# Kernel optimization log

Hardware: AMD Instinct MI355X
Metric: run time of the kernel (lower is better)

Reference implementation:

```python
import jax, jax.numpy as jnp
import numpy as np

HEADS = 8
HEAD_DIM = 64
INNER = HEADS * HEAD_DIM  # 512
DIM = 512
B, H, W = 8, 32, 32
KV_LEN, KV_DIM = 77, 1024


def group_norm(x, g, b, groups=32, eps=1e-6):
    # x: [B, C, H, W]
    Bx, C, Hx, Wx = x.shape
    xr = x.reshape(Bx, groups, C // groups, Hx, Wx)
    mu = xr.mean(axis=(2, 3, 4), keepdims=True)
    var = xr.var(axis=(2, 3, 4), keepdims=True)
    xr = (xr - mu) * jax.lax.rsqrt(var + eps)
    return xr.reshape(Bx, C, Hx, Wx) * g[None, :, None, None] + b[None, :, None, None]


def layer_norm(x, g, b, eps=1e-5):
    mu = x.mean(axis=-1, keepdims=True)
    var = x.var(axis=-1, keepdims=True)
    return (x - mu) * jax.lax.rsqrt(var + eps) * g + b


def attention(qx, kvx, Wq, Wk, Wv, Wo, bo):
    # qx: [B, Sq, dim_q], kvx: [B, Sk, dim_kv]
    q = qx @ Wq
    k = kvx @ Wk
    v = kvx @ Wv
    Bx, Sq, _ = q.shape
    Sk = k.shape[1]
    q = q.reshape(Bx, Sq, HEADS, HEAD_DIM)
    k = k.reshape(Bx, Sk, HEADS, HEAD_DIM)
    v = v.reshape(Bx, Sk, HEADS, HEAD_DIM)
    att = jnp.einsum('bqhd,bkhd->bhqk', q, k) * (HEAD_DIM ** -0.5)
    att = jax.nn.softmax(att.astype(jnp.float32), axis=-1).astype(q.dtype)
    o = jnp.einsum('bhqk,bkhd->bqhd', att, v).reshape(Bx, Sq, INNER)
    return o @ Wo + bo


def setup_inputs() -> dict:
    key = jax.random.key(0)
    ks = jax.random.split(key, 20)
    s = 0.02
    def n(k, shape):
        return jax.random.normal(k, shape, jnp.float32) * s
    return {
        'q': jax.random.normal(ks[0], (B, DIM, H, W), jnp.float32),
        'kv': jax.random.normal(ks[1], (B, KV_LEN, KV_DIM), jnp.float32),
        'gn_g': jnp.ones((DIM,), jnp.float32), 'gn_b': jnp.zeros((DIM,), jnp.float32),
        'ln2_g': jnp.ones((INNER,), jnp.float32), 'ln2_b': jnp.zeros((INNER,), jnp.float32),
        'ln3_g': jnp.ones((INNER,), jnp.float32), 'ln3_b': jnp.zeros((INNER,), jnp.float32),
        'ln4_g': jnp.ones((INNER,), jnp.float32), 'ln4_b': jnp.zeros((INNER,), jnp.float32),
        'fc_in_w': n(ks[2], (DIM, INNER)), 'fc_in_b': jnp.zeros((INNER,), jnp.float32),
        'fc_out_w': n(ks[3], (INNER, DIM)), 'fc_out_b': jnp.zeros((DIM,), jnp.float32),
        'a1_q': n(ks[4], (INNER, INNER)), 'a1_k': n(ks[5], (INNER, INNER)),
        'a1_v': n(ks[6], (INNER, INNER)), 'a1_o': n(ks[7], (INNER, INNER)),
        'a1_ob': jnp.zeros((INNER,), jnp.float32),
        'a2_q': n(ks[8], (INNER, INNER)), 'a2_k': n(ks[9], (KV_DIM, INNER)),
        'a2_v': n(ks[10], (KV_DIM, INNER)), 'a2_o': n(ks[11], (INNER, INNER)),
        'a2_ob': jnp.zeros((INNER,), jnp.float32),
        'ff_proj_w': n(ks[12], (INNER, INNER * 8)), 'ff_proj_b': jnp.zeros((INNER * 8,), jnp.float32),
        'ff_out_w': n(ks[13], (INNER * 4, INNER)), 'ff_out_b': jnp.zeros((INNER,), jnp.float32),
    }


def reference(q, kv, gn_g, gn_b, ln2_g, ln2_b, ln3_g, ln3_b, ln4_g, ln4_b,
              fc_in_w, fc_in_b, fc_out_w, fc_out_b,
              a1_q, a1_k, a1_v, a1_o, a1_ob,
              a2_q, a2_k, a2_v, a2_o, a2_ob,
              ff_proj_w, ff_proj_b, ff_out_w, ff_out_b):
    res = q
    Bx, C, Hx, Wx = q.shape
    x = group_norm(q, gn_g, gn_b)
    x = x.reshape(Bx, C, Hx * Wx).transpose(0, 2, 1)  # [B, S, C]
    x = x @ fc_in_w + fc_in_b
    t = layer_norm(x, ln2_g, ln2_b)
    x = attention(t, t, a1_q, a1_k, a1_v, a1_o, a1_ob) + x
    x = attention(layer_norm(x, ln3_g, ln3_b), kv, a2_q, a2_k, a2_v, a2_o, a2_ob) + x
    h = layer_norm(x, ln4_g, ln4_b) @ ff_proj_w + ff_proj_b
    a, gate = jnp.split(h, 2, axis=-1)
    x = (a * jax.nn.gelu(gate, approximate=False)) @ ff_out_w + ff_out_b + x
    x = x @ fc_out_w + fc_out_b
    x = x.transpose(0, 2, 1).reshape(Bx, C, Hx, Wx)
    return x + res
```

## Files before the change

### kernel.cpp

```cpp
#include <hip/hip_runtime.h>
#include <cstdint>
#include <cstddef>

typedef __attribute__((ext_vector_type(8))) short bf16x8;
typedef __attribute__((ext_vector_type(4))) short short4v;
typedef __attribute__((ext_vector_type(4))) float f32x4;

__device__ __forceinline__ short f2b(float f) {
    unsigned u = __builtin_bit_cast(unsigned, f);
    u = (u + 0x7FFFu + ((u >> 16) & 1u)) >> 16;
    return (short)u;
}
__device__ __forceinline__ float b2f(short s) {
    unsigned u = ((unsigned)(unsigned short)s) << 16;
    return __builtin_bit_cast(float, u);
}

__device__ __forceinline__ void gload16(const short* g, short* l) {
    __builtin_amdgcn_global_load_lds(
        (const __attribute__((address_space(1))) unsigned int*)g,
        (__attribute__((address_space(3))) unsigned int*)l, 16, 0, 0);
}

__device__ __forceinline__ float gelu_fast(float g) {
    float g2 = g * g;
    float gp = g * (0.7978845608f + 0.0356774081f * g2);
    float t = exp2f(-2.885390082f * gp);
    return g / (1.f + t);
}

__device__ __forceinline__ int pn_ffp(int n) {
    int m = (n < 2048) ? n : (n - 2048);
    int gofs = (n < 2048) ? 0 : 32;
    int x = m >> 6, c = m & 63;
    return x * 128 + ((c >> 5) << 6) + gofs + (c & 31);
}

struct PrepArgs {
    const float* src[12];
    short* dst[12];
    const float* kv;
    short* kvb;
    const float* fb;
    float* bp;
};

__global__ __launch_bounds__(256) void prep(PrepArgs a) {
    int t = blockIdx.x;
    int tid = threadIdx.x;
    if (t >= 6144) {
        if (t >= 6452) {
            int n = (t - 6452) * 256 + tid;
            if (n < 4096) a.bp[pn_ffp(n)] = a.fb[n];
            return;
        }
        int idx = (t - 6144) * 256 + tid;
        if (idx >= 78848) return;
        const float4* s = (const float4*)a.kv + (size_t)idx * 2;
        float4 va = s[0], vb = s[1];
        bf16x8 w;
        w[0] = f2b(va.x); w[1] = f2b(va.y); w[2] = f2b(va.z); w[3] = f2b(va.w);
        w[4] = f2b(vb.x); w[5] = f2b(vb.y); w[6] = f2b(vb.z); w[7] = f2b(vb.w);
        *(bf16x8*)(a.kvb + (size_t)idx * 8) = w;
        return;
    }
    const int jstart[12] = {0, 256, 512, 768, 1024, 1280, 1536, 1792, 2304, 2816, 3072, 5120};
    const int jK[12] = {512, 512, 512, 512, 512, 512, 512, 1024, 1024, 512, 512, 2048};
    const int jN[12] = {512, 512, 512, 512, 512, 512, 512, 512, 512, 512, 4096, 512};
    int j = 11;
#pragma unroll
    for (int i = 11; i >= 1; --i)
        if (t < jstart[i]) j = i - 1;
    int tx = t - jstart[j];
    int K = jK[j], N = jN[j];
    int tn = N >> 5;
    int n0 = (tx % tn) * 32, k0 = (tx / tn) * 32;
    const float* w = a.src[j];
    short* wt = a.dst[j];
    bool perm = (j == 10);

    __shared__ float tile[32][33];
    int cx = tid & 31, ty0 = tid >> 5;
#pragma unroll
    for (int i = 0; i < 4; ++i) {
        int r = ty0 + i * 8;
        tile[r][cx] = w[(size_t)(k0 + r) * N + n0 + cx];
    }
    __syncthreads();
    int r = tid >> 3;
    int kg = (tid & 7) * 4;
    int drow = perm ? pn_ffp(n0 + r) : (n0 + r);
    short4v o = {f2b(tile[kg][r]), f2b(tile[kg + 1][r]),
                 f2b(tile[kg + 2][r]), f2b(tile[kg + 3][r])};
    *(short4v*)&wt[(size_t)drow * K + k0 + kg] = o;
}

__global__ __launch_bounds__(256) void gn_stats(const float* __restrict__ q,
                                                const float* __restrict__ g,
                                                const float* __restrict__ bta,
                                                float* __restrict__ sc,
                                                float* __restrict__ sh) {
    int bb = blockIdx.x >> 5, gg = blockIdx.x & 31;
    const float4* src = (const float4*)(q + ((size_t)(bb * 512 + gg * 16)) * 1024);
    float s = 0.f, s2 = 0.f;
#pragma unroll
    for (int i = 0; i < 16; ++i) {
        float4 v = src[threadIdx.x + 256 * i];
        s += (v.x + v.y) + (v.z + v.w);
        s2 += (v.x * v.x + v.y * v.y) + (v.z * v.z + v.w * v.w);
    }
#pragma unroll
    for (int m = 1; m < 64; m <<= 1) {
        s += __shfl_xor(s, m);
        s2 += __shfl_xor(s2, m);
    }
    __shared__ float red[8];
    int wv = threadIdx.x >> 6;
    if ((threadIdx.x & 63) == 0) { red[wv] = s; red[4 + wv] = s2; }
    __syncthreads();
    if (threadIdx.x < 16) {
        float S = red[0] + red[1] + red[2] + red[3];
        float S2 = red[4] + red[5] + red[6] + red[7];
        float mu = S * (1.f / 16384.f);
        float var = S2 * (1.f / 16384.f) - mu * mu;
        float rs = rsqrtf(var + 1e-6f);
        int c = gg * 16 + threadIdx.x;
        float scale = rs * g[c];
        sc[bb * 512 + c] = scale;
        sh[bb * 512 + c] = bta[c] - mu * scale;
    }
}

__global__ __launch_bounds__(256) void gn_apply(const float* __restrict__ q,
                                                const float* __restrict__ sc,
                                                const float* __restrict__ sh,
                                                short* __restrict__ out) {
    __shared__ short tile[512][33];
    int b = blockIdx.x >> 5, st = blockIdx.x & 31;
    int s0 = st * 32;
    int sl = threadIdx.x & 31, cg = threadIdx.x >> 5;
    for (int c = cg; c < 512; c += 8) {
        float v = q[((size_t)(b * 512 + c)) * 1024 + s0 + sl];
        float y = v * sc[b * 512 + c] + sh[b * 512 + c];
        tile[c][sl] = f2b(y);
    }
    __syncthreads();
    int sr = threadIdx.x >> 3, ch = threadIdx.x & 7;
    short* orow = out + ((size_t)(b * 1024 + s0 + sr)) * 512;
    for (int c8 = ch * 64; c8 < ch * 64 + 64; c8 += 8) {
        bf16x8 o;
#pragma unroll
        for (int jj = 0; jj < 8; ++jj) o[jj] = tile[c8 + jj][sr];
        *(bf16x8*)&orow[c8] = o;
    }
}

__global__ __launch_bounds__(256) void ln_rows(const short* __restrict__ x,
                                               const float* __restrict__ g,
                                               const float* __restrict__ bta,
                                               short* __restrict__ out) {
    int row = blockIdx.x * 4 + (threadIdx.x >> 6);
    int lane = threadIdx.x & 63;
    bf16x8 v8 = *(const bf16x8*)(x + (size_t)row * 512 + lane * 8);
    float v[8];
#pragma unroll
    for (int j = 0; j < 8; ++j) v[j] = b2f(v8[j]);
    float s = 0.f, s2 = 0.f;
#pragma unroll
    for (int j = 0; j < 8; ++j) { s += v[j]; s2 += v[j] * v[j]; }
#pragma unroll
    for (int m = 1; m < 64; m <<= 1) {
        s += __shfl_xor(s, m);
        s2 += __shfl_xor(s2, m);
    }
    float mu = s * (1.f / 512.f);
    float var = s2 * (1.f / 512.f) - mu * mu;
    float rs = rsqrtf(var + 1e-5f);
    float4 ga = ((const float4*)g)[lane * 2], gb = ((const float4*)g)[lane * 2 + 1];
    float4 ba = ((const float4*)bta)[lane * 2], bb = ((const float4*)bta)[lane * 2 + 1];
    bf16x8 o;
    o[0] = f2b((v[0] - mu) * rs * ga.x + ba.x);
    o[1] = f2b((v[1] - mu) * rs * ga.y + ba.y);
    o[2] = f2b((v[2] - mu) * rs * ga.z + ba.z);
    o[3] = f2b((v[3] - mu) * rs * ga.w + ba.w);
    o[4] = f2b((v[4] - mu) * rs * gb.x + bb.x);
    o[5] = f2b((v[5] - mu) * rs * gb.y + bb.y);
    o[6] = f2b((v[6] - mu) * rs * gb.z + bb.z);
    o[7] = f2b((v[7] - mu) * rs * gb.w + bb.w);
    *(bf16x8*)(out + (size_t)row * 512 + lane * 8) = o;
}

template <int BN>
__global__ __launch_bounds__(256, 1) void gemm_gl(
    const short* __restrict__ A, const short* __restrict__ BT,
    int M, int N, int K,
    const float* __restrict__ bias,
    const short* __restrict__ addSrcB,
    short* __restrict__ outB,
    const float* __restrict__ resid,
    float* __restrict__ outFinal,
    int mode) {
    constexpr int FJ = BN / 32;
    constexpr int ASZ = 3 * 128 * 32;
    constexpr int BSZ = 3 * BN * 32;
    __shared__ __attribute__((aligned(16))) short smem[ASZ + BSZ];
    short* Asb = smem;
    short* Bsb = smem + ASZ;
    int tid = threadIdx.x;
    int wave = tid >> 6, lane = tid & 63;
    int wr = wave >> 1, wc = wave & 1;
    int m0 = blockIdx.y * 128, n0 = blockIdx.x * BN;
    f32x4 acc[4][FJ];
#pragma unroll
    for (int i = 0; i < 4; ++i)
#pragma unroll
        for (int j = 0; j < FJ; ++j) acc[i][j] = (f32x4){0.f, 0.f, 0.f, 0.f};

    int srow = tid >> 2;
    int scg = (((tid & 3) ^ ((tid >> 3) & 3)) << 3);
    int ar0 = m0 + srow; if (ar0 >= M) ar0 = M - 1;
    int ar1 = m0 + 64 + srow; if (ar1 >= M) ar1 = M - 1;
    const short* ag0 = A + (size_t)ar0 * K + scg;
    const short* ag1 = A + (size_t)ar1 * K + scg;
    const short* bg0 = BT + (size_t)(n0 + srow) * K + scg;
    const short* bg1 = BT + (size_t)(n0 + 64 + srow) * K + scg;
    int nk = K >> 5;

    auto stage = [&](int buf) {
        gload16(ag0, &Asb[buf * 4096 + wave * 512]);
        gload16(ag1, &Asb[buf * 4096 + 2048 + wave * 512]);
        gload16(bg0, &Bsb[buf * (BN * 32) + wave * 512]);
        if constexpr (BN == 128) gload16(bg1, &Bsb[buf * 4096 + 2048 + wave * 512]);
        ag0 += 32; ag1 += 32; bg0 += 32; bg1 += 32;
    };
    stage(0);
    stage(1);

    int lr = lane & 15, g = lane >> 4;

#define GL_STEP(KT, BUF)                                                          \
    {                                                                             \
        __builtin_amdgcn_sched_barrier(0);                                        \
        if ((KT) + 1 < nk) {                                                      \
            if constexpr (BN == 128)                                              \
                asm volatile("s_waitcnt vmcnt(4)" ::: "memory");                  \
            else                                                                  \
                asm volatile("s_waitcnt vmcnt(3)" ::: "memory");                  \
        } else {                                                                  \
            asm volatile("s_waitcnt vmcnt(0)" ::: "memory");                      \
        }                                                                         \
        __builtin_amdgcn_sched_barrier(0);                                        \
        __builtin_amdgcn_s_barrier();                                             \
        if ((KT) + 2 < nk) stage(((BUF) + 2) % 3);                                \
        bf16x8 af[4], bfr[FJ];                                                    \
        _Pragma("unroll") for (int i = 0; i < 4; ++i) {                           \
            int row = wr * 64 + i * 16 + lr;                                      \
            af[i] = *(const bf16x8*)&Asb[(BUF) * 4096 + row * 32 +                \
                                         ((g ^ ((row >> 1) & 3)) << 3)];          \
        }                                                                         \
        _Pragma("unroll") for (int j = 0; j < FJ; ++j) {                          \
            int row = wc * (BN / 2) + j * 16 + lr;                                \
            bfr[j] = *(const bf16x8*)&Bsb[(BUF) * (BN * 32) + row * 32 +          \
                                          ((g ^ ((row >> 1) & 3)) << 3)];         \
        }                                                                         \
        _Pragma("unroll") for (int i = 0; i < 4; ++i)                             \
            _Pragma("unroll") for (int j = 0; j < FJ; ++j)                        \
                acc[i][j] = __builtin_amdgcn_mfma_f32_16x16x32_bf16(              \
                    af[i], bfr[j], acc[i][j], 0, 0, 0);                           \
    }

    for (int kt = 0; kt < nk; kt += 3) {
        GL_STEP(kt, 0);
        if (kt + 1 < nk) GL_STEP(kt + 1, 1);
        if (kt + 2 < nk) GL_STEP(kt + 2, 2);
    }
#undef GL_STEP

    int lq = lane >> 4;
    if (mode == 1) {
#pragma unroll
        for (int i = 0; i < 4; ++i)
#pragma unroll
            for (int j = 0; j < FJ; ++j) {
                int mm0 = m0 + wr * 64 + i * 16 + lq * 4;
                int nn = n0 + wc * (BN / 2) + j * 16 + lr;
                int bb = mm0 >> 10, ss = mm0 & 1023;
                size_t oi = ((size_t)(bb * 512 + nn)) * 1024 + ss;
                float bv = bias ? bias[nn] : 0.f;
                float4 rv = *(const float4*)&resid[oi];
                float4 ov;
                ov.x = acc[i][j][0] + bv + rv.x;
                ov.y = acc[i][j][1] + bv + rv.y;
                ov.z = acc[i][j][2] + bv + rv.z;
                ov.w = acc[i][j][3] + bv + rv.w;
                *(float4*)&outFinal[oi] = ov;
            }
        return;
    }
    {
        constexpr int EC = BN + 4;
        float* ef = (float*)smem;
#pragma unroll
        for (int h = 0; h < 2; ++h) {
            __syncthreads();
            if (wr == h) {
#pragma unroll
                for (int i = 0; i < 4; ++i)
#pragma unroll
                    for (int j = 0; j < FJ; ++j)
#pragma unroll
                        for (int r = 0; r < 4; ++r)
                            ef[(i * 16 + lq * 4 + r) * EC + wc * (BN / 2) + j * 16 + lr] =
                                acc[i][j][r];
            }
            __syncthreads();
#pragma unroll
            for (int q = 0; q < BN / 16; ++q) {
                int idx = q * 256 + tid;
                int row = idx / (BN / 4);
                int cq = (idx % (BN / 4)) * 4;
                int mm = m0 + h * 64 + row;
                if (mm >= M) continue;
                int nn = n0 + cq;
                float4 v = *(float4*)&ef[row * EC + cq];
                if (bias) {
                    float4 b4 = *(const float4*)&bias[nn];
                    v.x += b4.x; v.y += b4.y; v.z += b4.z; v.w += b4.w;
                }
                size_t ig = (size_t)mm * N + nn;
                if (addSrcB) {
                    short4v a4 = *(const short4v*)&addSrcB[ig];
                    v.x += b2f(a4[0]); v.y += b2f(a4[1]);
                    v.z += b2f(a4[2]); v.w += b2f(a4[3]);
                }
                short4v o = {f2b(v.x), f2b(v.y), f2b(v.z), f2b(v.w)};
                *(short4v*)&outB[ig] = o;
            }
        }
    }
}

__global__ __launch_bounds__(512, 1) void gemm256w(
    const short* __restrict__ A, const short* __restrict__ BT,
    int M, int N, int K,
    const float* __restrict__ bias,
    const short* __restrict__ addSrcB,
    short* __restrict__ outB,
    int mode) {
    __shared__ __attribute__((aligned(16))) short smem[3 * 4096 + 3 * 8192];
    short* Asb = smem;
    short* Bsb = smem + 12288;
    int tid = threadIdx.x;
    int wave = tid >> 6, lane = tid & 63;
    int wrM = wave >> 2, wcN = wave & 3;
    int m0 = blockIdx.y * 128, n0 = blockIdx.x * 256;
    f32x4 acc[4][4];
#pragma unroll
    for (int i = 0; i < 4; ++i)
#pragma unroll
        for (int j = 0; j < 4; ++j) acc[i][j] = (f32x4){0.f, 0.f, 0.f, 0.f};

    const short* gp[3];
    int ldsoff[3];
    bool isA[3];
#pragma unroll
    for (int s = 0; s < 3; ++s) {
        int qq = wave * 3 + s;
        bool a = qq < 8;
        int r = (a ? qq : qq - 8) * 16 + (lane >> 2);
        int sc = (((lane & 3) ^ ((r >> 1) & 3)) << 3);
        gp[s] = a ? (A + (size_t)(m0 + r) * K + sc)
                  : (BT + (size_t)(n0 + r) * K + sc);
        ldsoff[s] = (a ? qq : (qq - 8)) * 512;
        isA[s] = a;
    }
    int nk = K >> 5;
    auto stage = [&](int buf) {
#pragma unroll
        for (int s = 0; s < 3; ++s) {
            short* l = isA[s] ? &Asb[buf * 4096 + ldsoff[s]]
                              : &Bsb[buf * 8192 + ldsoff[s]];
            gload16(gp[s], l);
            gp[s] += 32;
        }
    };
    stage(0);
    stage(1);

    int lr = lane & 15, g = lane >> 4;

#define W8_STEP(KT, BUF)                                                          \
    {                                                                             \
        __builtin_amdgcn_sched_barrier(0);                                        \
        if ((KT) + 1 < nk) {                                                      \
            asm volatile("s_waitcnt vmcnt(3)" ::: "memory");                      \
        } else {                                                                  \
            asm volatile("s_waitcnt vmcnt(0)" ::: "memory");                      \
        }                                                                         \
        __builtin_amdgcn_sched_barrier(0);                                        \
        __builtin_amdgcn_s_barrier();                                             \
        if ((KT) + 2 < nk) stage(((BUF) + 2) % 3);                                \
        bf16x8 af[4], bfr[4];                                                     \
        _Pragma("unroll") for (int i = 0; i < 4; ++i) {                           \
            int row = wrM * 64 + i * 16 + lr;                                     \
            af[i] = *(const bf16x8*)&Asb[(BUF) * 4096 + row * 32 +                \
                                         ((g ^ ((row >> 1) & 3)) << 3)];          \
        }                                                                         \
        _Pragma("unroll") for (int j = 0; j < 4; ++j) {                           \
            int row = wcN * 64 + j * 16 + lr;                                     \
            bfr[j] = *(const bf16x8*)&Bsb[(BUF) * 8192 + row * 32 +               \
                                          ((g ^ ((row >> 1) & 3)) << 3)];         \
        }                                                                         \
        _Pragma("unroll") for (int i = 0; i < 4; ++i)                             \
            _Pragma("unroll") for (int j = 0; j < 4; ++j)                         \
                acc[i][j] = __builtin_amdgcn_mfma_f32_16x16x32_bf16(              \
                    af[i], bfr[j], acc[i][j], 0, 0, 0);                           \
    }

    for (int kt = 0; kt < nk; kt += 3) {
        W8_STEP(kt, 0);
        if (kt + 1 < nk) W8_STEP(kt + 1, 1);
        if (kt + 2 < nk) W8_STEP(kt + 2, 2);
    }
#undef W8_STEP

    int lq = lane >> 4;
    if (mode == 2) {
        short* eb = smem;
        int xhalf = wcN >> 1, half = wcN & 1;
        __syncthreads();
#pragma unroll
        for (int i = 0; i < 4; ++i)
#pragma unroll
            for (int j = 0; j < 2; ++j)
#pragma unroll
                for (int r = 0; r < 4; ++r) {
                    int slot = n0 + wcN * 64 + j * 16 + lr;
                    float a = acc[i][j][r] + bias[slot];
                    float gt = acc[i][j + 2][r] + bias[slot + 32];
                    float ge = gelu_fast(gt);
                    int row = wrM * 64 + i * 16 + lq * 4 + r;
                    int col = xhalf * 64 + half * 32 + j * 16 + lr;
                    eb[row * 136 + col] = f2b(a * ge);
                }
        __syncthreads();
#pragma unroll
        for (int q = 0; q < 4; ++q) {
            int idx = q * 512 + tid;
            int row = idx >> 4, cg = (idx & 15) * 8;
            bf16x8 o = *(bf16x8*)&eb[row * 136 + cg];
            *(bf16x8*)&outB[(size_t)(m0 + row) * 2048 + blockIdx.x * 128 + cg] = o;
        }
        return;
    }
    {
        float* ef = (float*)smem;
#pragma unroll
        for (int h = 0; h < 2; ++h) {
            __syncthreads();
            if (wrM == h) {
#pragma unroll
                for (int i = 0; i < 4; ++i)
#pragma unroll
                    for (int j = 0; j < 4; ++j)
#pragma unroll
                        for (int r = 0; r < 4; ++r)
                            ef[(i * 16 + lq * 4 + r) * 260 + wcN * 64 + j * 16 + lr] =
                                acc[i][j][r];
            }
            __syncthreads();
#pragma unroll
            for (int q = 0; q < 8; ++q) {
                int idx = q * 512 + tid;
                int row = idx >> 6;
                int cq = (idx & 63) * 4;
                float4 v = *(float4*)&ef[row * 260 + cq];
                int nn = n0 + cq;
                if (bias) {
                    float4 b4 = *(const float4*)&bias[nn];
                    v.x += b4.x; v.y += b4.y; v.z += b4.z; v.w += b4.w;
                }
                size_t ig = (size_t)(m0 + h * 64 + row) * N + nn;
                if (addSrcB) {
                    short4v a4 = *(const short4v*)&addSrcB[ig];
                    v.x += b2f(a4[0]); v.y += b2f(a4[1]);
                    v.z += b2f(a4[2]); v.w += b2f(a4[3]);
                }
                short4v o = {f2b(v.x), f2b(v.y), f2b(v.z), f2b(v.w)};
                *(short4v*)&outB[ig] = o;
            }
        }
    }
}

__global__ __launch_bounds__(256, 1) void attn_mfma(const short* __restrict__ qp,
                                                    const short* __restrict__ kp,
                                                    const short* __restrict__ vp,
                                                    short* __restrict__ op,
                                                    int kv_len, int kvBatchRows,
                                                    int qStride, int kvStride) {
    __shared__ __attribute__((aligned(16))) short Kt[64][72];
    __shared__ __attribute__((aligned(16))) short Vt[64][72];
    __shared__ __attribute__((aligned(16))) short Pt[4][2][16][72];
    int tid = threadIdx.x, w = tid >> 6, lane = tid & 63;
    int g = lane >> 4, c = lane & 15;
    int id = blockIdx.x;
    int xcd = id & 7, jj2 = id >> 3;
    int bh = xcd * 8 + (jj2 >> 3);
    int qtile = jj2 & 7;
    int b = bh >> 3, h = bh & 7;
    int q0 = qtile * 128 + w * 16;

    const float QS = 0.125f * 1.44269504f;
    bf16x8 qa[2][2];
#pragma unroll
    for (int qi = 0; qi < 2; ++qi) {
        const short* qbase = qp + ((size_t)(b * 1024 + q0 + qi * 64 + c)) * qStride + h * 64;
        bf16x8 qr0 = *(const bf16x8*)(qbase + g * 8);
        bf16x8 qr1 = *(const bf16x8*)(qbase + 32 + g * 8);
#pragma unroll
        for (int j = 0; j < 8; ++j) {
            qa[qi][0][j] = f2b(b2f(qr0[j]) * QS);
            qa[qi][1][j] = f2b(b2f(qr1[j]) * QS);
        }
    }

    f32x4 oac[2][4];
#pragma unroll
    for (int qi = 0; qi < 2; ++qi)
#pragma unroll
        for (int dt = 0; dt < 4; ++dt) oac[qi][dt] = (f32x4){0.f, 0.f, 0.f, 0.f};
    float l[2][4];
#pragma unroll
    for (int qi = 0; qi < 2; ++qi)
#pragma unroll
        for (int r = 0; r < 4; ++r) l[qi][r] = 0.f;

    int skey = tid & 63, sd0 = (tid >> 6) * 16;
    int ntile = (kv_len + 63) >> 6;
    size_t kvbase = (size_t)b * kvBatchRows;

    bf16x8 k0, k1, v0, v1;
    {
        int krow = skey < kv_len ? skey : kv_len - 1;
        const short* kpp = kp + (kvbase + krow) * kvStride + h * 64 + sd0;
        const short* vpp = vp + (kvbase + krow) * kvStride + h * 64 + sd0;
        k0 = *(const bf16x8*)kpp; k1 = *(const bf16x8*)(kpp + 8);
        v0 = *(const bf16x8*)vpp; v1 = *(const bf16x8*)(vpp + 8);
    }

    for (int kt = 0; kt < ntile; ++kt) {
        __syncthreads();
        *(bf16x8*)&Kt[skey][sd0] = k0;
        *(bf16x8*)&Kt[skey][sd0 + 8] = k1;
#pragma unroll
        for (int j = 0; j < 8; ++j) {
            Vt[sd0 + j][skey] = v0[j];
            Vt[sd0 + 8 + j][skey] = v1[j];
        }
        __syncthreads();
        if (kt + 1 < ntile) {
            int krow = (kt + 1) * 64 + skey;
            if (krow >= kv_len) krow = kv_len - 1;
            const short* kpp = kp + (kvbase + krow) * kvStride + h * 64 + sd0;
            const short* vpp = vp + (kvbase + krow) * kvStride + h * 64 + sd0;
            k0 = *(const bf16x8*)kpp; k1 = *(const bf16x8*)(kpp + 8);
            v0 = *(const bf16x8*)vpp; v1 = *(const bf16x8*)(vpp + 8);
        }

        f32x4 s[2][4];
        __builtin_amdgcn_s_setprio(1);
#pragma unroll
        for (int nt = 0; nt < 4; ++nt) {
            bf16x8 kb0 = *(const bf16x8*)&Kt[nt * 16 + c][g * 8];
            bf16x8 kb1 = *(const bf16x8*)&Kt[nt * 16 + c][32 + g * 8];
#pragma unroll
            for (int qi = 0; qi < 2; ++qi) {
                s[qi][nt] = __builtin_amdgcn_mfma_f32_16x16x32_bf16(
                    qa[qi][0], kb0, (f32x4){0.f, 0.f, 0.f, 0.f}, 0, 0, 0);
                s[qi][nt] = __builtin_amdgcn_mfma_f32_16x16x32_bf16(
                    qa[qi][1], kb1, s[qi][nt], 0, 0, 0);
            }
        }
        __builtin_amdgcn_s_setprio(0);
        if (kt * 64 + 64 > kv_len) {
#pragma unroll
            for (int nt = 0; nt < 4; ++nt) {
                bool valid = kt * 64 + nt * 16 + c < kv_len;
#pragma unroll
                for (int qi = 0; qi < 2; ++qi)
#pragma unroll
                    for (int r = 0; r < 4; ++r) {
                        float pv = valid ? exp2f(s[qi][nt][r]) : 0.f;
                        s[qi][nt][r] = pv;
                        l[qi][r] += pv;
                    }
            }
        } else {
#pragma unroll
            for (int nt = 0; nt < 4; ++nt)
#pragma unroll
                for (int qi = 0; qi < 2; ++qi)
#pragma unroll
                    for (int r = 0; r < 4; ++r) {
                        float pv = exp2f(s[qi][nt][r]);
                        s[qi][nt][r] = pv;
                        l[qi][r] += pv;
                    }
        }

        bf16x8 pa[2][2];
#pragma unroll
        for (int qi = 0; qi < 2; ++qi) {
#pragma unroll
            for (int nt = 0; nt < 4; ++nt)
#pragma unroll
                for (int r = 0; r < 4; ++r)
                    Pt[w][qi][4 * g + r][nt * 16 + c] = f2b(s[qi][nt][r]);
        }
#pragma unroll
        for (int qi = 0; qi < 2; ++qi) {
            pa[qi][0] = *(const bf16x8*)&Pt[w][qi][c][g * 8];
            pa[qi][1] = *(const bf16x8*)&Pt[w][qi][c][32 + g * 8];
        }
        __builtin_amdgcn_s_setprio(1);
#pragma unroll
        for (int dt = 0; dt < 4; ++dt) {
            bf16x8 vb0 = *(const bf16x8*)&Vt[dt * 16 + c][g * 8];
            bf16x8 vb1 = *(const bf16x8*)&Vt[dt * 16 + c][32 + g * 8];
#pragma unroll
            for (int qi = 0; qi < 2; ++qi) {
                oac[qi][dt] = __builtin_amdgcn_mfma_f32_16x16x32_bf16(pa[qi][0], vb0, oac[qi][dt], 0, 0, 0);
                oac[qi][dt] = __builtin_amdgcn_mfma_f32_16x16x32_bf16(pa[qi][1], vb1, oac[qi][dt], 0, 0, 0);
            }
        }
        __builtin_amdgcn_s_setprio(0);
    }

#pragma unroll
    for (int mk = 1; mk < 16; mk <<= 1)
#pragma unroll
        for (int qi = 0; qi < 2; ++qi)
#pragma unroll
            for (int r = 0; r < 4; ++r) l[qi][r] += __shfl_xor(l[qi][r], mk);
#pragma unroll
    for (int qi = 0; qi < 2; ++qi)
#pragma unroll
        for (int r = 0; r < 4; ++r) {
            float inv = 1.f / l[qi][r];
            short* orow = op + ((size_t)(b * 1024 + q0 + qi * 64 + 4 * g + r)) * 512 + h * 64;
#pragma unroll
            for (int dt = 0; dt < 4; ++dt)
                orow[dt * 16 + c] = f2b(oac[qi][dt][r] * inv);
        }
}

extern "C" void kernel_launch(void* const* d_in, const int* in_sizes, int n_in,
                              void* d_out, int out_size, void* d_ws, size_t ws_size,
                              hipStream_t stream) {
    (void)in_sizes; (void)n_in; (void)out_size; (void)ws_size;
    const float* q_in = (const float*)d_in[0];
    const float* kv_in = (const float*)d_in[1];
    const float* gn_g = (const float*)d_in[2];
    const float* gn_b = (const float*)d_in[3];
    const float* ln2_g = (const float*)d_in[4];
    const float* ln2_b = (const float*)d_in[5];
    const float* ln3_g = (const float*)d_in[6];
    const float* ln3_b = (const float*)d_in[7];
    const float* ln4_g = (const float*)d_in[8];
    const float* ln4_b = (const float*)d_in[9];
    const float* fc_in_w = (const float*)d_in[10];
    const float* fc_in_b = (const float*)d_in[11];
    const float* fc_out_w = (const float*)d_in[12];
    const float* fc_out_b = (const float*)d_in[13];
    const float* a1_qw = (const float*)d_in[14];
    const float* a1_kw = (const float*)d_in[15];
    const float* a1_vw = (const float*)d_in[16];
    const float* a1_ow = (const float*)d_in[17];
    const float* a1_ob = (const float*)d_in[18];
    const float* a2_qw = (const float*)d_in[19];
    const float* a2_kw = (const float*)d_in[20];
    const float* a2_vw = (const float*)d_in[21];
    const float* a2_ow = (const float*)d_in[22];
    const float* a2_ob = (const float*)d_in[23];
    const float* ffp_w = (const float*)d_in[24];
    const float* ffp_b = (const float*)d_in[25];
    const float* ffo_w = (const float*)d_in[26];
    const float* ffo_b = (const float*)d_in[27];
    float* out = (float*)d_out;

    char* p = (char*)d_ws;
    auto alloc = [&](size_t n) {
        char* r = p;
        p += (n + 255) & ~(size_t)255;
        return r;
    };
    short* wt_fci = (short*)alloc((size_t)512 * 512 * 2);
    short* wt_fco = (short*)alloc((size_t)512 * 512 * 2);
    short* wt_qkv = (short*)alloc((size_t)1536 * 512 * 2);
    short* wt_a1o = (short*)alloc((size_t)512 * 512 * 2);
    short* wt_a2q = (short*)alloc((size_t)512 * 512 * 2);
    short* wt_kv2 = (short*)alloc((size_t)1024 * 1024 * 2);
    short* wt_a2o = (short*)alloc((size_t)512 * 512 * 2);
    short* wt_ffp = (short*)alloc((size_t)4096 * 512 * 2);
    short* wt_ffo = (short*)alloc((size_t)512 * 2048 * 2);
    float* biasP = (float*)alloc((size_t)4096 * 4);
    short* xb = (short*)alloc((size_t)8192 * 512 * 2);
    short* tb = (short*)alloc((size_t)8192 * 512 * 2);
    short* qkvbuf = (short*)alloc((size_t)8192 * 1536 * 2);
    short* qbuf = (short*)alloc((size_t)8192 * 512 * 2);
    short* kvpbuf = (short*)alloc((size_t)616 * 1024 * 2);
    short* obuf = (short*)alloc((size_t)8192 * 512 * 2);
    short* kvb = (short*)alloc((size_t)616 * 1024 * 2);
    short* ggb = (short*)alloc((size_t)8192 * 2048 * 2);
    float* gnsc = (float*)alloc((size_t)8 * 512 * 4);
    float* gnsh = (float*)alloc((size_t)8 * 512 * 4);

    PrepArgs pa;
    pa.src[0] = fc_in_w;  pa.dst[0] = wt_fci;
    pa.src[1] = fc_out_w; pa.dst[1] = wt_fco;
    pa.src[2] = a1_qw;    pa.dst[2] = wt_qkv;
    pa.src[3] = a1_kw;    pa.dst[3] = wt_qkv + (size_t)512 * 512;
    pa.src[4] = a1_vw;    pa.dst[4] = wt_qkv + (size_t)1024 * 512;
    pa.src[5] = a1_ow;    pa.dst[5] = wt_a1o;
    pa.src[6] = a2_qw;    pa.dst[6] = wt_a2q;
    pa.src[7] = a2_kw;    pa.dst[7] = wt_kv2;
    pa.src[8] = a2_vw;    pa.dst[8] = wt_kv2 + (size_t)512 * 1024;
    pa.src[9] = a2_ow;    pa.dst[9] = wt_a2o;
    pa.src[10] = ffp_w;   pa.dst[10] = wt_ffp;
    pa.src[11] = ffo_w;   pa.dst[11] = wt_ffo;
    pa.kv = kv_in; pa.kvb = kvb; pa.fb = ffp_b; pa.bp = biasP;
    prep<<<6468, 256, 0, stream>>>(pa);

    auto gemm128n = [&](const short* A, const short* BT, int M, int N, int K,
                        const float* bias, const short* addSrcB, short* outB,
                        const float* resid, float* outFinal, int mode) {
        dim3 g(N / 128, (M + 127) / 128);
        gemm_gl<128><<<g, 256, 0, stream>>>(A, BT, M, N, K, bias, addSrcB, outB,
                                            resid, outFinal, mode);
    };

    gn_stats<<<256, 256, 0, stream>>>(q_in, gn_g, gn_b, gnsc, gnsh);
    gn_apply<<<256, 256, 0, stream>>>(q_in, gnsc, gnsh, tb);
    gemm128n(tb, wt_fci, 8192, 512, 512, fc_in_b, nullptr, xb, nullptr, nullptr, 0);
    ln_rows<<<2048, 256, 0, stream>>>(xb, ln2_g, ln2_b, tb);
    gemm256w<<<dim3(6, 64), 512, 0, stream>>>(tb, wt_qkv, 8192, 1536, 512,
                                              nullptr, nullptr, qkvbuf, 0);
    attn_mfma<<<512, 256, 0, stream>>>(qkvbuf, qkvbuf + 512, qkvbuf + 1024, obuf,
                                       1024, 1024, 1536, 1536);
    gemm128n(obuf, wt_a1o, 8192, 512, 512, a1_ob, xb, xb, nullptr, nullptr, 0);
    ln_rows<<<2048, 256, 0, stream>>>(xb, ln3_g, ln3_b, tb);
    gemm128n(tb, wt_a2q, 8192, 512, 512, nullptr, nullptr, qbuf, nullptr, nullptr, 0);
    gemm128n(kvb, wt_kv2, 616, 1024, 1024, nullptr, nullptr, kvpbuf, nullptr, nullptr, 0);
    attn_mfma<<<512, 256, 0, stream>>>(qbuf, kvpbuf, kvpbuf + 512, obuf,
                                       77, 77, 512, 1024);
    gemm128n(obuf, wt_a2o, 8192, 512, 512, a2_ob, xb, xb, nullptr, nullptr, 0);
    ln_rows<<<2048, 256, 0, stream>>>(xb, ln4_g, ln4_b, tb);
    gemm256w<<<dim3(16, 64), 512, 0, stream>>>(tb, wt_ffp, 8192, 4096, 512,
                                               biasP, nullptr, ggb, 2);
    gemm256w<<<dim3(2, 64), 512, 0, stream>>>(ggb, wt_ffo, 8192, 512, 2048,
                                              ffo_b, xb, tb, 0);
    gemm128n(tb, wt_fco, 8192, 512, 512, fc_out_b, nullptr, nullptr, q_in, out, 1);
}
```

Baseline: 294.6 us.

## Fold GN stats into prep, template GEMM K, compute softmax sum via MFMA

The group-norm statistics kernel is merged into the prep launch as extra blocks, which removes one kernel launch. The GEMM kernels now take K as a template parameter and fully unroll the k-loop, so the compiler can specialize addressing. In attention, the per-row softmax denominator is now accumulated with extra MFMAs against a vector of bf16 ones, replacing scalar adds and cross-lane shuffles. The denominator is then summed from bf16-rounded probabilities, and the fully unrolled loops increase code size.

```diff
diff --git a/kernel.cpp b/kernel.cpp
--- a/kernel.cpp
+++ b/kernel.cpp
@@ -43,12 +43,50 @@
     short* kvb;
     const float* fb;
     float* bp;
+    const float* qin;
+    const float* gng;
+    const float* gnb;
+    float* gnsc;
+    float* gnsh;
 };
 
 __global__ __launch_bounds__(256) void prep(PrepArgs a) {
     int t = blockIdx.x;
     int tid = threadIdx.x;
+    __shared__ float tile[32][33];
     if (t >= 6144) {
+        if (t >= 6468) {
+            int bb = (t - 6468) >> 5, gg = (t - 6468) & 31;
+            const float4* src = (const float4*)(a.qin + ((size_t)(bb * 512 + gg * 16)) * 1024);
+            float s = 0.f, s2 = 0.f;
+#pragma unroll
+            for (int i = 0; i < 16; ++i) {
+                float4 v = src[tid + 256 * i];
+                s += (v.x + v.y) + (v.z + v.w);
+                s2 += (v.x * v.x + v.y * v.y) + (v.z * v.z + v.w * v.w);
+            }
+#pragma unroll
+            for (int m = 1; m < 64; m <<= 1) {
+                s += __shfl_xor(s, m);
+                s2 += __shfl_xor(s2, m);
+            }
+            float* red = &tile[0][0];
+            int wv = tid >> 6;
+            if ((tid & 63) == 0) { red[wv] = s; red[4 + wv] = s2; }
+            __syncthreads();
+            if (tid < 16) {
+                float S = red[0] + red[1] + red[2] + red[3];
+                float S2 = red[4] + red[5] + red[6] + red[7];
+                float mu = S * (1.f / 16384.f);
+                float var = S2 * (1.f / 16384.f) - mu * mu;
+                float rs = rsqrtf(var + 1e-6f);
+                int c = gg * 16 + tid;
+                float scale = rs * a.gng[c];
+                a.gnsc[bb * 512 + c] = scale;
+                a.gnsh[bb * 512 + c] = a.gnb[c] - mu * scale;
+            }
+            return;
+        }
         if (t >= 6452) {
             int n = (t - 6452) * 256 + tid;
             if (n < 4096) a.bp[pn_ffp(n)] = a.fb[n];
@@ -79,7 +117,6 @@
     short* wt = a.dst[j];
     bool perm = (j == 10);
 
-    __shared__ float tile[32][33];
     int cx = tid & 31, ty0 = tid >> 5;
 #pragma unroll
     for (int i = 0; i < 4; ++i) {
@@ -93,42 +130,6 @@
     short4v o = {f2b(tile[kg][r]), f2b(tile[kg + 1][r]),
                  f2b(tile[kg + 2][r]), f2b(tile[kg + 3][r])};
     *(short4v*)&wt[(size_t)drow * K + k0 + kg] = o;
-}
-
-__global__ __launch_bounds__(256) void gn_stats(const float* __restrict__ q,
-                                                const float* __restrict__ g,
-                                                const float* __restrict__ bta,
-                                                float* __restrict__ sc,
-                                                float* __restrict__ sh) {
-    int bb = blockIdx.x >> 5, gg = blockIdx.x & 31;
-    const float4* src = (const float4*)(q + ((size_t)(bb * 512 + gg * 16)) * 1024);
-    float s = 0.f, s2 = 0.f;
-#pragma unroll
-    for (int i = 0; i < 16; ++i) {
-        float4 v = src[threadIdx.x + 256 * i];
-        s += (v.x + v.y) + (v.z + v.w);
-        s2 += (v.x * v.x + v.y * v.y) + (v.z * v.z + v.w * v.w);
-    }
-#pragma unroll
-    for (int m = 1; m < 64; m <<= 1) {
-        s += __shfl_xor(s, m);
-        s2 += __shfl_xor(s2, m);
-    }
-    __shared__ float red[8];
-    int wv = threadIdx.x >> 6;
-    if ((threadIdx.x & 63) == 0) { red[wv] = s; red[4 + wv] = s2; }
-    __syncthreads();
-    if (threadIdx.x < 16) {
-        float S = red[0] + red[1] + red[2] + red[3];
-        float S2 = red[4] + red[5] + red[6] + red[7];
-        float mu = S * (1.f / 16384.f);
-        float var = S2 * (1.f / 16384.f) - mu * mu;
-        float rs = rsqrtf(var + 1e-6f);
-        int c = gg * 16 + threadIdx.x;
-        float scale = rs * g[c];
-        sc[bb * 512 + c] = scale;
-        sh[bb * 512 + c] = bta[c] - mu * scale;
-    }
 }
 
 __global__ __launch_bounds__(256) void gn_apply(const float* __restrict__ q,
@@ -190,10 +191,10 @@
     *(bf16x8*)(out + (size_t)row * 512 + lane * 8) = o;
 }
 
-template <int BN>
+template <int BN, int KK>
 __global__ __launch_bounds__(256, 1) void gemm_gl(
     const short* __restrict__ A, const short* __restrict__ BT,
-    int M, int N, int K,
+    int M, int N,
     const float* __restrict__ bias,
     const short* __restrict__ addSrcB,
     short* __restrict__ outB,
@@ -201,6 +202,8 @@
     float* __restrict__ outFinal,
     int mode) {
     constexpr int FJ = BN / 32;
+    constexpr int K = KK;
+    constexpr int nk = KK / 32;
     constexpr int ASZ = 3 * 128 * 32;
     constexpr int BSZ = 3 * BN * 32;
     __shared__ __attribute__((aligned(16))) short smem[ASZ + BSZ];
@@ -224,7 +227,6 @@
     const short* ag1 = A + (size_t)ar1 * K + scg;
     const short* bg0 = BT + (size_t)(n0 + srow) * K + scg;
     const short* bg1 = BT + (size_t)(n0 + 64 + srow) * K + scg;
-    int nk = K >> 5;
 
     auto stage = [&](int buf) {
         gload16(ag0, &Asb[buf * 4096 + wave * 512]);
@@ -269,6 +271,7 @@
                     af[i], bfr[j], acc[i][j], 0, 0, 0);                           \
     }
 
+#pragma unroll
     for (int kt = 0; kt < nk; kt += 3) {
         GL_STEP(kt, 0);
         if (kt + 1 < nk) GL_STEP(kt + 1, 1);
@@ -340,13 +343,16 @@
     }
 }
 
+template <int KK>
 __global__ __launch_bounds__(512, 1) void gemm256w(
     const short* __restrict__ A, const short* __restrict__ BT,
-    int M, int N, int K,
+    int M, int N,
     const float* __restrict__ bias,
     const short* __restrict__ addSrcB,
     short* __restrict__ outB,
     int mode) {
+    constexpr int K = KK;
+    constexpr int nk = KK / 32;
     __shared__ __attribute__((aligned(16))) short smem[3 * 4096 + 3 * 8192];
     short* Asb = smem;
     short* Bsb = smem + 12288;
@@ -374,7 +380,6 @@
         ldsoff[s] = (a ? qq : (qq - 8)) * 512;
         isA[s] = a;
     }
-    int nk = K >> 5;
     auto stage = [&](int buf) {
 #pragma unroll
         for (int s = 0; s < 3; ++s) {
@@ -417,6 +422,7 @@
                     af[i], bfr[j], acc[i][j], 0, 0, 0);                           \
     }
 
+#pragma unroll
     for (int kt = 0; kt < nk; kt += 3) {
         W8_STEP(kt, 0);
         if (kt + 1 < nk) W8_STEP(kt + 1, 1);
@@ -524,17 +530,17 @@
             qa[qi][1][j] = f2b(b2f(qr1[j]) * QS);
         }
     }
-
-    f32x4 oac[2][4];
-#pragma unroll
-    for (int qi = 0; qi < 2; ++qi)
+    bf16x8 vones;
+#pragma unroll
+    for (int j = 0; j < 8; ++j) vones[j] = (short)0x3F80;
+
+    f32x4 oac[2][4], oacl[2];
+#pragma unroll
+    for (int qi = 0; qi < 2; ++qi) {
 #pragma unroll
         for (int dt = 0; dt < 4; ++dt) oac[qi][dt] = (f32x4){0.f, 0.f, 0.f, 0.f};
-    float l[2][4];
-#pragma unroll
-    for (int qi = 0; qi < 2; ++qi)
-#pragma unroll
-        for (int r = 0; r < 4; ++r) l[qi][r] = 0.f;
+        oacl[qi] = (f32x4){0.f, 0.f, 0.f, 0.f};
+    }
 
     int skey = tid & 63, sd0 = (tid >> 6) * 16;
     int ntile = (kv_len + 63) >> 6;
@@ -590,11 +596,8 @@
 #pragma unroll
                 for (int qi = 0; qi < 2; ++qi)
 #pragma unroll
-                    for (int r = 0; r < 4; ++r) {
-                        float pv = valid ? exp2f(s[qi][nt][r]) : 0.f;
-                        s[qi][nt][r] = pv;
-                        l[qi][r] += pv;
-                    }
+                    for (int r = 0; r < 4; ++r)
+                        s[qi][nt][r] = valid ? exp2f(s[qi][nt][r]) : 0.f;
             }
         } else {
 #pragma unroll
@@ -602,11 +605,8 @@
 #pragma unroll
                 for (int qi = 0; qi < 2; ++qi)
 #pragma unroll
-                    for (int r = 0; r < 4; ++r) {
-                        float pv = exp2f(s[qi][nt][r]);
-                        s[qi][nt][r] = pv;
-                        l[qi][r] += pv;
-                    }
+                    for (int r = 0; r < 4; ++r)
+                        s[qi][nt][r] = exp2f(s[qi][nt][r]);
         }
 
         bf16x8 pa[2][2];
@@ -634,20 +634,19 @@
                 oac[qi][dt] = __builtin_amdgcn_mfma_f32_16x16x32_bf16(pa[qi][1], vb1, oac[qi][dt], 0, 0, 0);
             }
         }
+#pragma unroll
+        for (int qi = 0; qi < 2; ++qi) {
+            oacl[qi] = __builtin_amdgcn_mfma_f32_16x16x32_bf16(pa[qi][0], vones, oacl[qi], 0, 0, 0);
+            oacl[qi] = __builtin_amdgcn_mfma_f32_16x16x32_bf16(pa[qi][1], vones, oacl[qi], 0, 0, 0);
+        }
         __builtin_amdgcn_s_setprio(0);
     }
 
 #pragma unroll
-    for (int mk = 1; mk < 16; mk <<= 1)
-#pragma unroll
-        for (int qi = 0; qi < 2; ++qi)
-#pragma unroll
-            for (int r = 0; r < 4; ++r) l[qi][r] += __shfl_xor(l[qi][r], mk);
-#pragma unroll
     for (int qi = 0; qi < 2; ++qi)
 #pragma unroll
         for (int r = 0; r < 4; ++r) {
-            float inv = 1.f / l[qi][r];
+            float inv = 1.f / oacl[qi][r];
             short* orow = op + ((size_t)(b * 1024 + q0 + qi * 64 + 4 * g + r)) * 512 + h * 64;
 #pragma unroll
             for (int dt = 0; dt < 4; ++dt)
@@ -730,35 +729,33 @@
     pa.src[10] = ffp_w;   pa.dst[10] = wt_ffp;
     pa.src[11] = ffo_w;   pa.dst[11] = wt_ffo;
     pa.kv = kv_in; pa.kvb = kvb; pa.fb = ffp_b; pa.bp = biasP;
-    prep<<<6468, 256, 0, stream>>>(pa);
-
-    auto gemm128n = [&](const short* A, const short* BT, int M, int N, int K,
-                        const float* bias, const short* addSrcB, short* outB,
-                        const float* resid, float* outFinal, int mode) {
-        dim3 g(N / 128, (M + 127) / 128);
-        gemm_gl<128><<<g, 256, 0, stream>>>(A, BT, M, N, K, bias, addSrcB, outB,
-                                            resid, outFinal, mode);
-    };
-
-    gn_stats<<<256, 256, 0, stream>>>(q_in, gn_g, gn_b, gnsc, gnsh);
+    pa.qin = q_in; pa.gng = gn_g; pa.gnb = gn_b; pa.gnsc = gnsc; pa.gnsh = gnsh;
+    prep<<<6724, 256, 0, stream>>>(pa);
+
     gn_apply<<<256, 256, 0, stream>>>(q_in, gnsc, gnsh, tb);
-    gemm128n(tb, wt_fci, 8192, 512, 512, fc_in_b, nullptr, xb, nullptr, nullptr, 0);
+    gemm_gl<128, 512><<<dim3(4, 64), 256, 0, stream>>>(
+        tb, wt_fci, 8192, 512, fc_in_b, nullptr, xb, nullptr, nullptr, 0);
     ln_rows<<<2048, 256, 0, stream>>>(xb, ln2_g, ln2_b, tb);
-    gemm256w<<<dim3(6, 64), 512, 0, stream>>>(tb, wt_qkv, 8192, 1536, 512,
-                                              nullptr, nullptr, qkvbuf, 0);
+    gemm256w<512><<<dim3(6, 64), 512, 0, stream>>>(tb, wt_qkv, 8192, 1536,
+                                                   nullptr, nullptr, qkvbuf, 0);
     attn_mfma<<<512, 256, 0, stream>>>(qkvbuf, qkvbuf + 512, qkvbuf + 1024, obuf,
                                        1024, 1024, 1536, 1536);
-    gemm128n(obuf, wt_a1o, 8192, 512, 512, a1_ob, xb, xb, nullptr, nullptr, 0);
+    gemm_gl<128, 512><<<dim3(4, 64), 256, 0, stream>>>(
+        obuf, wt_a1o, 8192, 512, a1_ob, xb, xb, nullptr, nullptr, 0);
     ln_rows<<<2048, 256, 0, stream>>>(xb, ln3_g, ln3_b, tb);
-    gemm128n(tb, wt_a2q, 8192, 512, 512, nullptr, nullptr, qbuf, nullptr, nullptr, 0);
-    gemm128n(kvb, wt_kv2, 616, 1024, 1024, nullptr, nullptr, kvpbuf, nullptr, nullptr, 0);
+    gemm_gl<128, 512><<<dim3(4, 64), 256, 0, stream>>>(
+        tb, wt_a2q, 8192, 512, nullptr, nullptr, qbuf, nullptr, nullptr, 0);
+    gemm_gl<128, 1024><<<dim3(8, 5), 256, 0, stream>>>(
+        kvb, wt_kv2, 616, 1024, nullptr, nullptr, kvpbuf, nullptr, nullptr, 0);
     attn_mfma<<<512, 256, 0, stream>>>(qbuf, kvpbuf, kvpbuf + 512, obuf,
                                        77, 77, 512, 1024);
-    gemm128n(obuf, wt_a2o, 8192, 512, 512, a2_ob, xb, xb, nullptr, nullptr, 0);
+    gemm_gl<128, 512><<<dim3(4, 64), 256, 0, stream>>>(
+        obuf, wt_a2o, 8192, 512, a2_ob, xb, xb, nullptr, nullptr, 0);
     ln_rows<<<2048, 256, 0, stream>>>(xb, ln4_g, ln4_b, tb);
-    gemm256w<<<dim3(16, 64), 512, 0, stream>>>(tb, wt_ffp, 8192, 4096, 512,
-                                               biasP, nullptr, ggb, 2);
-    gemm256w<<<dim3(2, 64), 512, 0, stream>>>(ggb, wt_ffo, 8192, 512, 2048,
-                                              ffo_b, xb, tb, 0);
-    gemm128n(tb, wt_fco, 8192, 512, 512, fc_out_b, nullptr, nullptr, q_in, out, 1);
-}
+    gemm256w<512><<<dim3(16, 64), 512, 0, stream>>>(tb, wt_ffp, 8192, 4096,
+                                                    biasP, nullptr, ggb, 2);
+    gemm256w<2048><<<dim3(2, 64), 512, 0, stream>>>(ggb, wt_ffo, 8192, 512,
+                                                    ffo_b, xb, tb, 0);
+    gemm_gl<128, 512><<<dim3(4, 64), 256, 0, stream>>>(
+        tb, wt_fco, 8192, 512, fc_out_b, nullptr, nullptr, q_in, out, 1);
+}
```

New measurement: 290.5 us. No clear change (-1.4%).
